# Performance work log

Measured on AMD Instinct MI355X. Metric: run time of the kernel, lower is better.

Reference implementation:

```python
import jax, jax.numpy as jnp
import numpy as np

EPS = 1e-6
CHUNK = 128  # chunk size for the causal linear-attention scan


def elu_plus_one(x):
    return jax.nn.elu(x) + 1.0


def causal_linear_attention(q, k, v):
    # out_t = (sq_t @ cumsum_{j<=t} sk_j v_j^T) / (sq_t . cumsum_{j<=t} sk_j), clamped
    B, S, D = q.shape
    sq = elu_plus_one(q)
    sk = elu_plus_one(k)
    N = S // CHUNK
    # [N, B, C, D] chunked layout for scan over chunks
    sq_c = sq.reshape(B, N, CHUNK, D).transpose(1, 0, 2, 3)
    sk_c = sk.reshape(B, N, CHUNK, D).transpose(1, 0, 2, 3)
    v_c = v.reshape(B, N, CHUNK, D).transpose(1, 0, 2, 3)
    mask = jnp.tril(jnp.ones((CHUNK, CHUNK), dtype=q.dtype))  # inclusive causal

    def step(carry, inp):
        S_kv, z = carry  # [B,D,D], [B,D] running sums from previous chunks
        sqi, ski, vi = inp
        A = jnp.einsum('bid,bjd->bij', sqi, ski) * mask  # intra-chunk causal scores
        num = jnp.einsum('bij,bje->bie', A, vi) + jnp.einsum('bid,bde->bie', sqi, S_kv)
        den = A.sum(-1) + jnp.einsum('bid,bd->bi', sqi, z)
        out = num / jnp.clip(den, EPS, None)[..., None]
        S_kv = S_kv + jnp.einsum('bcd,bce->bde', ski, vi)
        z = z + ski.sum(axis=1)
        return (S_kv, z), out

    init = (jnp.zeros((B, D, D), q.dtype), jnp.zeros((B, D), q.dtype))
    _, outs = jax.lax.scan(step, init, (sq_c, sk_c, v_c))
    return outs.transpose(1, 0, 2, 3).reshape(B, S, D)


def setup_inputs() -> dict:
    key = jax.random.key(0)
    ks = jax.random.split(key, 8)
    B, S, D = 2, 2048, 1024
    scale = 1.0 / np.sqrt(D)  # realistic init scale for the D x D projections
    return {
        'hidden_states': jax.random.normal(ks[0], (B, S, D), jnp.float32),
        'w_q': jax.random.normal(ks[1], (D, D), jnp.float32) * scale,
        'w_k': jax.random.normal(ks[2], (D, D), jnp.float32) * scale,
        'w_v': jax.random.normal(ks[3], (D, D), jnp.float32) * scale,
        'w_o': jax.random.normal(ks[4], (D, D), jnp.float32) * scale,
        'gate': jnp.zeros((1,), jnp.float32),
        'memory': jax.random.uniform(ks[5], (D, D), jnp.float32) * 0.01,
        'memory_norm': jax.random.uniform(ks[6], (D,), jnp.float32),
    }


def reference(hidden_states, w_q, w_k, w_v, w_o, gate, memory, memory_norm):
    # Projections (torch Linear: x @ W^T)
    q = hidden_states @ w_q.T
    k = hidden_states @ w_k.T
    v = hidden_states @ w_v.T

    # Retrieve from compressive memory (single bank)
    sigma_q = elu_plus_one(q)
    a_mem = sigma_q @ memory
    norm = jnp.clip(sigma_q @ memory_norm, EPS, None)[..., None]
    active = (memory_norm.sum() >= EPS).astype(q.dtype)
    memory_output = active * (a_mem / norm)

    local_output = causal_linear_attention(q, k, v)

    g = jax.nn.sigmoid(gate)  # [1], broadcasts
    output = g * memory_output + (1.0 - g) * local_output
    return output @ w_o.T
```

## Files before the change

kernel.cpp:

```cpp
#include <hip/hip_runtime.h>
#include <cstddef>

#define EPSF 1e-6f

constexpr int D   = 1024;
constexpr int Bv  = 2;
constexpr int S   = 2048;
constexpr int M   = Bv * S;
constexpr int CH  = 256;
constexpr int NCH = S / CH;

constexpr int TSZ  = 128 * 32;
constexpr int TA64 = 64 * 32;

typedef __attribute__((ext_vector_type(8))) short short8;
typedef __attribute__((ext_vector_type(4))) float floatx4;

__device__ __forceinline__ float elu1(float x) { return x > 0.f ? x + 1.f : __expf(x); }
__device__ __forceinline__ float sigmoidf_(float x) { return 1.f / (1.f + __expf(-x)); }
__device__ __forceinline__ unsigned short f2bf(float x) {
    unsigned u = __float_as_uint(x);
    return (unsigned short)((u + 0x7fffu + ((u >> 16) & 1u)) >> 16);
}
__device__ __forceinline__ float bf2f(unsigned short h) {
    return __uint_as_float(((unsigned)h) << 16);
}
__device__ __forceinline__ float wave_reduce(float x) {
#pragma unroll
    for (int off = 32; off > 0; off >>= 1) x += __shfl_down(x, off);
    return x;
}

__device__ __forceinline__ void gl_lds16(const unsigned short* g, unsigned short* l) {
    __builtin_amdgcn_global_load_lds(
        (const __attribute__((address_space(1))) void*)g,
        (__attribute__((address_space(3))) void*)l, 16, 0, 0);
}

__device__ __forceinline__ void stage128x32(const unsigned short* g, int stride,
                                            unsigned short* lds, int wave, int lane) {
    const int t   = (wave << 6) + lane;
    const int row = t >> 2;
    const int cb  = (((t & 3) ^ ((row >> 1) & 3)) << 3);
    unsigned short* l0 = lds + (wave << 9);
    gl_lds16(g + (size_t)row * stride + cb, l0);
    gl_lds16(g + (size_t)(row + 64) * stride + cb, l0 + 2048);
}

__device__ __forceinline__ void stage64x32(const unsigned short* g, int stride,
                                           unsigned short* lds, int wave, int lane) {
    const int t   = (wave << 6) + lane;
    const int row = t >> 2;
    const int cb  = (((t & 3) ^ ((row >> 1) & 3)) << 3);
    gl_lds16(g + (size_t)row * stride + cb, lds + (wave << 9));
}

__device__ __forceinline__ void mfma_step(const unsigned short* As, const unsigned short* Bs,
                                          int wm, int wn, int fr, int g, floatx4 acc[4][4]) {
    const int off = ((g ^ ((fr >> 1) & 3)) << 3);
    short8 af[4], bf[4];
#pragma unroll
    for (int i = 0; i < 4; ++i) af[i] = *(const short8*)&As[(wm + i * 16 + fr) * 32 + off];
#pragma unroll
    for (int j = 0; j < 4; ++j) bf[j] = *(const short8*)&Bs[(wn + j * 16 + fr) * 32 + off];
#pragma unroll
    for (int i = 0; i < 4; ++i)
#pragma unroll
        for (int j = 0; j < 4; ++j)
            acc[i][j] = __builtin_amdgcn_mfma_f32_16x16x32_bf16(af[i], bf[j], acc[i][j], 0, 0, 0);
}

__device__ __forceinline__ void mfma_step64d(const unsigned short* As, const unsigned short* Bs,
                                             int wm, int wn, int fr, int g,
                                             floatx4 acc[2][4], floatx4 accd[2], short8 bones) {
    const int off = ((g ^ ((fr >> 1) & 3)) << 3);
    short8 af[2], bf[4];
#pragma unroll
    for (int i = 0; i < 2; ++i) af[i] = *(const short8*)&As[(wm + i * 16 + fr) * 32 + off];
#pragma unroll
    for (int j = 0; j < 4; ++j) bf[j] = *(const short8*)&Bs[(wn + j * 16 + fr) * 32 + off];
#pragma unroll
    for (int i = 0; i < 2; ++i) {
#pragma unroll
        for (int j = 0; j < 4; ++j)
            acc[i][j] = __builtin_amdgcn_mfma_f32_16x16x32_bf16(af[i], bf[j], acc[i][j], 0, 0, 0);
        accd[i] = __builtin_amdgcn_mfma_f32_16x16x32_bf16(af[i], bones, accd[i], 0, 0, 0);
    }
}

__device__ __forceinline__ void mfma_step64(const unsigned short* As, const unsigned short* Bs,
                                            int wm, int wn, int fr, int g, floatx4 acc[2][4]) {
    const int off = ((g ^ ((fr >> 1) & 3)) << 3);
    short8 af[2], bf[4];
#pragma unroll
    for (int i = 0; i < 2; ++i) af[i] = *(const short8*)&As[(wm + i * 16 + fr) * 32 + off];
#pragma unroll
    for (int j = 0; j < 4; ++j) bf[j] = *(const short8*)&Bs[(wn + j * 16 + fr) * 32 + off];
#pragma unroll
    for (int i = 0; i < 2; ++i)
#pragma unroll
        for (int j = 0; j < 4; ++j)
            acc[i][j] = __builtin_amdgcn_mfma_f32_16x16x32_bf16(af[i], bf[j], acc[i][j], 0, 0, 0);
}

__device__ __forceinline__ void gemm_loop_db(const unsigned short* Ag, int strideA,
                                             const unsigned short* Bg, int strideB, int Kk,
                                             unsigned short* As, unsigned short* Bs,
                                             int wave, int lane, int wm, int wn, int fr, int g,
                                             floatx4 acc[4][4]) {
    __syncthreads();
    stage128x32(Ag, strideA, As, wave, lane);
    stage128x32(Bg, strideB, Bs, wave, lane);
    int buf = 0;
    for (int k0 = 32; k0 < Kk; k0 += 32) {
        __syncthreads();
        const int nb = buf ^ 1;
        stage128x32(Ag + k0, strideA, As + nb * TSZ, wave, lane);
        stage128x32(Bg + k0, strideB, Bs + nb * TSZ, wave, lane);
        mfma_step(As + buf * TSZ, Bs + buf * TSZ, wm, wn, fr, g, acc);
        buf = nb;
    }
    __syncthreads();
    mfma_step(As + buf * TSZ, Bs + buf * TSZ, wm, wn, fr, g, acc);
}

__device__ __forceinline__ void gemm_loop_db64d(const unsigned short* Ag, int strideA,
                                                const unsigned short* Bg, int strideB, int Kk,
                                                unsigned short* As, unsigned short* Bs,
                                                int wave, int lane, int wm, int wn, int fr, int g,
                                                floatx4 acc[2][4], floatx4 accd[2], short8 bones) {
    __syncthreads();
    stage64x32(Ag, strideA, As, wave, lane);
    stage128x32(Bg, strideB, Bs, wave, lane);
    int buf = 0;
    for (int k0 = 32; k0 < Kk; k0 += 32) {
        __syncthreads();
        const int nb = buf ^ 1;
        stage64x32(Ag + k0, strideA, As + nb * TA64, wave, lane);
        stage128x32(Bg + k0, strideB, Bs + nb * TSZ, wave, lane);
        mfma_step64d(As + buf * TA64, Bs + buf * TSZ, wm, wn, fr, g, acc, accd, bones);
        buf = nb;
    }
    __syncthreads();
    mfma_step64d(As + buf * TA64, Bs + buf * TSZ, wm, wn, fr, g, acc, accd, bones);
}

__device__ __forceinline__ void gemm_loop_db64(const unsigned short* Ag, int strideA,
                                               const unsigned short* Bg, int strideB, int Kk,
                                               unsigned short* As, unsigned short* Bs,
                                               int wave, int lane, int wm, int wn, int fr, int g,
                                               floatx4 acc[2][4]) {
    __syncthreads();
    stage64x32(Ag, strideA, As, wave, lane);
    stage128x32(Bg, strideB, Bs, wave, lane);
    int buf = 0;
    for (int k0 = 32; k0 < Kk; k0 += 32) {
        __syncthreads();
        const int nb = buf ^ 1;
        stage64x32(Ag + k0, strideA, As + nb * TA64, wave, lane);
        stage128x32(Bg + k0, strideB, Bs + nb * TSZ, wave, lane);
        mfma_step64(As + buf * TA64, Bs + buf * TSZ, wm, wn, fr, g, acc);
        buf = nb;
    }
    __syncthreads();
    mfma_step64(As + buf * TA64, Bs + buf * TSZ, wm, wn, fr, g, acc);
}

__global__ __launch_bounds__(256) void prep(const float* __restrict__ h,
                                            const float* __restrict__ w_q, const float* __restrict__ w_k,
                                            const float* __restrict__ w_v, const float* __restrict__ w_o,
                                            const float* __restrict__ memory,
                                            unsigned short* __restrict__ h_b,
                                            unsigned short* __restrict__ wq_b, unsigned short* __restrict__ wk_b,
                                            unsigned short* __restrict__ wv_b, unsigned short* __restrict__ wo_b,
                                            unsigned short* __restrict__ memT)
{
    __shared__ unsigned short T[64][72];
    const int id = blockIdx.x, tid = threadIdx.x;
    if (id < 4096) {
        const size_t i = ((size_t)id * 256 + tid) * 4;
        float4 v = *(const float4*)(h + i);
        ushort4 o; o.x = f2bf(v.x); o.y = f2bf(v.y); o.z = f2bf(v.z); o.w = f2bf(v.w);
        *(ushort4*)(h_b + i) = o;
    } else if (id < 8192) {
        const int t = id - 4096, which = t >> 10;
        const float* in = (which == 0) ? w_q : (which == 1) ? w_k : (which == 2) ? w_v : w_o;
        unsigned short* out = (which == 0) ? wq_b : (which == 1) ? wk_b : (which == 2) ? wv_b : wo_b;
        const size_t i = ((size_t)(t & 1023) * 256 + tid) * 4;
        float4 v = *(const float4*)(in + i);
        ushort4 o; o.x = f2bf(v.x); o.y = f2bf(v.y); o.z = f2bf(v.z); o.w = f2bf(v.w);
        *(ushort4*)(out + i) = o;
    } else {
        const int t = id - 8192;
        const int d0 = (t >> 4) * 64, e0 = (t & 15) * 64;
        const int r = tid >> 4, c4 = (tid & 15) * 4;
        for (int rr = r; rr < 64; rr += 16) {
            float4 v = *(const float4*)(memory + (size_t)(d0 + rr) * D + e0 + c4);
            T[rr][c4 + 0] = f2bf(v.x); T[rr][c4 + 1] = f2bf(v.y);
            T[rr][c4 + 2] = f2bf(v.z); T[rr][c4 + 3] = f2bf(v.w);
        }
        __syncthreads();
        for (int rr = r; rr < 64; rr += 16) {
            ushort4 o;
            o.x = T[c4 + 0][rr]; o.y = T[c4 + 1][rr];
            o.z = T[c4 + 2][rr]; o.w = T[c4 + 3][rr];
            *(ushort4*)(memT + (size_t)(e0 + rr) * D + d0 + c4) = o;
        }
    }
}

__global__ __launch_bounds__(512, 2) void proj8(const unsigned short* __restrict__ h_b,
                                                const unsigned short* __restrict__ wq,
                                                const unsigned short* __restrict__ wk,
                                                const unsigned short* __restrict__ wv,
                                                unsigned short* __restrict__ sq,
                                                unsigned short* __restrict__ sk,
                                                unsigned short* __restrict__ v)
{
    extern __shared__ unsigned short sm[];
    const int id = blockIdx.x;
    const int x = id & 7, y = id >> 3;
    const int strip = x + 8 * (y % 6);
    const int nn = y / 6;
    const int sub = strip >> 4, m = strip & 15;
    const int m0 = m * 256, n0 = nn * 256;
    const unsigned short* Ag = h_b + (size_t)m0 * D;
    const unsigned short* Bg = ((sub == 0) ? wq : (sub == 1) ? wk : wv) + (size_t)n0 * D;
    unsigned short* C = (sub == 0) ? sq : (sub == 1) ? sk : v;

    const int tid = threadIdx.x;
    const int w = tid >> 6, lane = tid & 63;
    const int wr = w >> 2, wc = w & 3;
    const int fr = lane & 15, gq = lane >> 4;
    const int swz = fr & 7;

    const int r0 = tid >> 3;
    const int c0 = (tid & 7) ^ (r0 & 7);
    const int r1 = (tid + 512) >> 3;
    const int c1 = ((tid + 512) & 7) ^ (r1 & 7);
    const size_t so0 = (size_t)r0 * D + (size_t)c0 * 8;
    const size_t so1 = (size_t)r1 * D + (size_t)c1 * 8;
    unsigned short* const dst0 = sm + tid * 8;
    unsigned short* const dst1 = sm + (tid + 512) * 8;

    floatx4 acc[8][4] = {};

#define STG(kt, b, which) do {                                                      \
        const unsigned short* Gs = ((which) < 2 ? Ag : Bg)                          \
            + (size_t)(((which) & 1) * 128) * D + (size_t)(kt) * 64;                \
        const int slot = (((b) << 2) + (which)) << 13;                              \
        gl_lds16(Gs + so0, dst0 + slot);                                            \
        gl_lds16(Gs + so1, dst1 + slot);                                            \
    } while (0)

    STG(0, 0, 0); STG(0, 0, 1); STG(0, 0, 2); STG(0, 0, 3);
    STG(1, 1, 2); STG(1, 1, 3);
    asm volatile("s_waitcnt vmcnt(4)" ::: "memory");
    __builtin_amdgcn_s_barrier();

    const int NT = D / 64;
    for (int u = 0; u < NT; ++u) {
        const int bu = u & 1;
        const unsigned short* Ah = sm + (((bu << 2) + wr) << 13);
        const unsigned short* Bh = sm + (((bu << 2) + 2 + (wc >> 1)) << 13);
        const int brow = (wc & 1) * 64;
        short8 bfr[4][2];
#pragma unroll
        for (int s = 0; s < 4; ++s) {
            short8 afr[2][2];
#pragma unroll
            for (int i2 = 0; i2 < 2; ++i2)
#pragma unroll
                for (int ks = 0; ks < 2; ++ks)
                    afr[i2][ks] = *(const short8*)&Ah[((s * 2 + i2) * 16 + fr) * 64
                                                      + ((((ks << 2) + gq) ^ swz) << 3)];
            if (s == 0) {
#pragma unroll
                for (int j = 0; j < 4; ++j)
#pragma unroll
                    for (int ks = 0; ks < 2; ++ks)
                        bfr[j][ks] = *(const short8*)&Bh[(brow + j * 16 + fr) * 64
                                                         + ((((ks << 2) + gq) ^ swz) << 3)];
            }
            if (s == 0)      { if (u + 1 < NT) STG(u + 1, bu ^ 1, 0); }
            else if (s == 1) { if (u + 1 < NT) STG(u + 1, bu ^ 1, 1); }
            else if (s == 2) { if (u + 2 < NT) STG(u + 2, bu, 2); }
            else {
                if (u + 2 < NT) {
                    STG(u + 2, bu, 3);
                    asm volatile("s_waitcnt vmcnt(4)" ::: "memory");
                } else if (u + 1 < NT) {
                    asm volatile("s_waitcnt vmcnt(0)" ::: "memory");
                }
            }
            __builtin_amdgcn_s_barrier();
            __builtin_amdgcn_s_setprio(1);
#pragma unroll
            for (int i2 = 0; i2 < 2; ++i2)
#pragma unroll
                for (int j = 0; j < 4; ++j)
#pragma unroll
                    for (int ks = 0; ks < 2; ++ks)
                        acc[s * 2 + i2][j] = __builtin_amdgcn_mfma_f32_16x16x32_bf16(
                            afr[i2][ks], bfr[j][ks], acc[s * 2 + i2][j], 0, 0, 0);
            __builtin_amdgcn_s_setprio(0);
            __builtin_amdgcn_s_barrier();
        }
    }
#undef STG

    const int q4 = gq * 4;
#pragma unroll
    for (int i = 0; i < 8; ++i)
#pragma unroll
        for (int j = 0; j < 4; ++j) {
            const int col = n0 + wc * 64 + j * 16 + fr;
#pragma unroll
            for (int r = 0; r < 4; ++r) {
                const int row = m0 + wr * 128 + i * 16 + q4 + r;
                float val = acc[i][j][r];
                if (sub < 2) val = elu1(val);
                C[(size_t)row * D + col] = f2bf(val);
            }
        }
}

__global__ __launch_bounds__(256) void proj_fused(const unsigned short* __restrict__ h_b,
                                                  const unsigned short* __restrict__ wq,
                                                  const unsigned short* __restrict__ wk,
                                                  const unsigned short* __restrict__ wv,
                                                  unsigned short* __restrict__ sq,
                                                  unsigned short* __restrict__ sk,
                                                  unsigned short* __restrict__ v)
{
    __shared__ unsigned short As[2 * TSZ], Bs[2 * TSZ];
    const int id = blockIdx.x;
    const int x = id & 7, y = id >> 3;
    const int strip = x + 8 * (y % 12);
    const int n     = y / 12;
    const int sub = strip >> 5, m = strip & 31;
    const int m0 = m * 128, n0 = n * 128;
    const unsigned short* B = (sub == 0) ? wq : (sub == 1) ? wk : wv;
    unsigned short* C = (sub == 0) ? sq : (sub == 1) ? sk : v;

    const int tid = threadIdx.x, wave = tid >> 6, lane = tid & 63;
    const int wm = (wave >> 1) * 64, wn = (wave & 1) * 64;
    const int fr = lane & 15, g = lane >> 4;
    const int q4 = g * 4;

    floatx4 acc[4][4] = {};
    gemm_loop_db(h_b + (size_t)m0 * D, D, B + (size_t)n0 * D, D, D,
                 As, Bs, wave, lane, wm, wn, fr, g, acc);

#pragma unroll
    for (int i = 0; i < 4; ++i)
#pragma unroll
        for (int j = 0; j < 4; ++j) {
            const int col = n0 + wn + j * 16 + fr;
#pragma unroll
            for (int r = 0; r < 4; ++r) {
                const int row = m0 + wm + i * 16 + q4 + r;
                float val = acc[i][j][r];
                if (sub < 2) val = elu1(val);
                C[(size_t)row * D + col] = f2bf(val);
            }
        }
}

__global__ __launch_bounds__(256) void stage2(const unsigned short* __restrict__ sq,
                                              const unsigned short* __restrict__ sk,
                                              const unsigned short* __restrict__ memT,
                                              const unsigned short* __restrict__ v_b,
                                              const float* __restrict__ mnorm,
                                              const float* __restrict__ gate,
                                              unsigned short* __restrict__ combm,
                                              unsigned short* __restrict__ Sbuf2,
                                              unsigned short* __restrict__ vT,
                                              float* __restrict__ rowscale)
{
    __shared__ unsigned short As[2 * TSZ], Bs[2 * TSZ];
    const int id = blockIdx.x, tid = threadIdx.x;
    const int wave = tid >> 6, lane = tid & 63;
    const int wm = (wave >> 1) * 64, wn = (wave & 1) * 64;
    const int fr = lane & 15, g = lane >> 4;
    const int q4 = g * 4;

    if (id < 256) {
        const int x = id & 7, y = id >> 3;
        const int m0 = (x + 8 * (y & 3)) * 128;
        const int n0 = (y >> 2) * 128;
        floatx4 acc[4][4] = {};
        gemm_loop_db(sq + (size_t)m0 * D, D, memT + (size_t)n0 * D, D, D,
                     As, Bs, wave, lane, wm, wn, fr, g, acc);
#pragma unroll
        for (int i = 0; i < 4; ++i)
#pragma unroll
            for (int j = 0; j < 4; ++j) {
                const int col = n0 + wn + j * 16 + fr;
#pragma unroll
                for (int r = 0; r < 4; ++r)
                    combm[(size_t)(m0 + wm + i * 16 + q4 + r) * D + col] = f2bf(acc[i][j][r]);
            }
    } else if (id < 544) {
        const int t = id - 256;
        const int b = t / 144, rem = t % 144;
        const int p = rem >> 2, tt = rem & 3;
        const int it = tt >> 1, jt = tt & 1;
        int c = 0;
        while ((c + 1) * (c + 2) / 2 <= p) ++c;
        const int j = p - c * (c + 1) / 2;
        unsigned short* Srow0 = Sbuf2 + (size_t)(b * NCH + c) * CH * S;

        if (j == c && jt > it) {
            const int row = it * 128 + (tid >> 1);
            unsigned short* zp = Srow0 + (size_t)row * S + j * CH + jt * 128 + (tid & 1) * 64;
            uint4 z4 = make_uint4(0, 0, 0, 0);
#pragma unroll
            for (int i = 0; i < 8; ++i) *(uint4*)(zp + i * 8) = z4;
            return;
        }
        floatx4 acc[4][4] = {};
        gemm_loop_db(sq + ((size_t)b * S + (size_t)c * CH + it * 128) * D, D,
                     sk + ((size_t)b * S + (size_t)j * CH + jt * 128) * D, D, D,
                     As, Bs, wave, lane, wm, wn, fr, g, acc);
        const bool diag = (j == c && it == jt);
#pragma unroll
        for (int i = 0; i < 4; ++i)
#pragma unroll
            for (int jj = 0; jj < 4; ++jj) {
                const int col = jt * 128 + wn + jj * 16 + fr;
#pragma unroll
                for (int r = 0; r < 4; ++r) {
                    const int row = it * 128 + wm + i * 16 + q4 + r;
                    float val = acc[i][jj][r];
                    if (diag && col > row) val = 0.f;
                    Srow0[(size_t)row * S + j * CH + col] = f2bf(val);
                }
            }
    } else if (id < 1568) {
        unsigned short (*T)[72] = (unsigned short(*)[72])As;
        const int t = id - 544;
        const int b = t >> 9, rem = t & 511;
        const int s0 = (rem >> 4) * 64, d0 = (rem & 15) * 64;
        const int r = tid >> 4, c4 = (tid & 15) * 4;
        const unsigned short* ip = v_b + (size_t)b * S * D;
        for (int rr = r; rr < 64; rr += 16) {
            ushort4 vv = *(const ushort4*)(ip + (size_t)(s0 + rr) * D + d0 + c4);
            T[rr][c4 + 0] = vv.x; T[rr][c4 + 1] = vv.y; T[rr][c4 + 2] = vv.z; T[rr][c4 + 3] = vv.w;
        }
        __syncthreads();
        unsigned short* op = vT + (size_t)b * D * S;
        for (int rr = r; rr < 64; rr += 16) {
            ushort4 o;
            o.x = T[c4 + 0][rr]; o.y = T[c4 + 1][rr];
            o.z = T[c4 + 2][rr]; o.w = T[c4 + 3][rr];
            *(ushort4*)(op + (size_t)(d0 + rr) * S + s0 + c4) = o;
        }
    } else {
        const int row = (id - 1568) * 4 + wave;
        const unsigned short* sr = sq + (size_t)row * D;
        float dot = 0.f, msum = 0.f;
#pragma unroll
        for (int p = 0; p < 2; ++p) {
            const int d0 = p * 512 + lane * 8;
            short8 sv = *(const short8*)(sr + d0);
            float4 m0 = *(const float4*)(mnorm + d0);
            float4 m1 = *(const float4*)(mnorm + d0 + 4);
            dot += bf2f((unsigned short)sv[0]) * m0.x + bf2f((unsigned short)sv[1]) * m0.y
                 + bf2f((unsigned short)sv[2]) * m0.z + bf2f((unsigned short)sv[3]) * m0.w
                 + bf2f((unsigned short)sv[4]) * m1.x + bf2f((unsigned short)sv[5]) * m1.y
                 + bf2f((unsigned short)sv[6]) * m1.z + bf2f((unsigned short)sv[7]) * m1.w;
            msum += m0.x + m0.y + m0.z + m0.w + m1.x + m1.y + m1.z + m1.w;
        }
        dot = wave_reduce(dot);
        msum = wave_reduce(msum);
        if (lane == 0) {
            const float gg = sigmoidf_(gate[0]);
            const float active = (msum >= EPSF) ? 1.f : 0.f;
            rowscale[row] = gg * active / fmaxf(dot, EPSF);
        }
    }
}

__global__ __launch_bounds__(256) void pv64(const unsigned short* __restrict__ Sbuf2,
                                            const unsigned short* __restrict__ vT,
                                            const float* __restrict__ rowscale,
                                            const float* __restrict__ gate,
                                            unsigned short* __restrict__ combm)
{
    __shared__ unsigned short As2[2 * TA64], Bs2[2 * TSZ];
    const int id = blockIdx.x, tid = threadIdx.x;
    const int wave = tid >> 6, lane = tid & 63;
    const int wm = (wave >> 1) * 32, wn = (wave & 1) * 64;
    const int fr = lane & 15, g = lane >> 4;
    const int q4 = g * 4;

    const int x = id & 7, y = id >> 3;
    const int g_ = x + 8 * (y & 7);
    const int e  = y >> 3;
    const int b = g_ >> 5;
    const int rem = g_ & 31;
    const int c = (NCH - 1) - (rem >> 2);
    const int i0 = (rem & 3) * 64, e0 = e * 128;

    const short one_bf = (short)0x3F80;
    short8 bones = {one_bf, one_bf, one_bf, one_bf, one_bf, one_bf, one_bf, one_bf};

    floatx4 acc[2][4] = {};
    floatx4 accd[2] = {};
    gemm_loop_db64d(Sbuf2 + ((size_t)(b * NCH + c) * CH + i0) * S, S,
                    vT + (size_t)b * D * S + (size_t)e0 * S, S, (c + 1) * CH,
                    As2, Bs2, wave, lane, wm, wn, fr, g, acc, accd, bones);

    const float gg = sigmoidf_(gate[0]);
    const float wloc = 1.f - gg;
#pragma unroll
    for (int i = 0; i < 2; ++i)
#pragma unroll
        for (int j = 0; j < 4; ++j) {
            const int col = e0 + wn + j * 16 + fr;
#pragma unroll
            for (int r = 0; r < 4; ++r) {
                const int li = i0 + wm + i * 16 + q4 + r;
                const int rg = b * S + c * CH + li;
                const float inv = wloc / fmaxf(accd[i][r], EPSF);
                const size_t idx = (size_t)rg * D + col;
                combm[idx] = f2bf(bf2f(combm[idx]) * rowscale[rg] + acc[i][j][r] * inv);
            }
        }
}

__global__ __launch_bounds__(256) void outproj64(const unsigned short* __restrict__ A,
                                                 const unsigned short* __restrict__ wo,
                                                 float* __restrict__ out)
{
    __shared__ unsigned short As2[2 * TA64], Bs2[2 * TSZ];
    const int id = blockIdx.x, tid = threadIdx.x;
    const int wave = tid >> 6, lane = tid & 63;
    const int wm = (wave >> 1) * 32, wn = (wave & 1) * 64;
    const int fr = lane & 15, g = lane >> 4;
    const int q4 = g * 4;

    const int x = id & 7, y = id >> 3;
    const int m0 = (x + 8 * (y & 7)) * 64;
    const int n0 = (y >> 3) * 128;

    floatx4 acc[2][4] = {};
    gemm_loop_db64(A + (size_t)m0 * D, D, wo + (size_t)n0 * D, D, D,
                   As2, Bs2, wave, lane, wm, wn, fr, g, acc);

#pragma unroll
    for (int i = 0; i < 2; ++i)
#pragma unroll
        for (int j = 0; j < 4; ++j) {
            const int col = n0 + wn + j * 16 + fr;
#pragma unroll
            for (int r = 0; r < 4; ++r)
                out[(size_t)(m0 + wm + i * 16 + q4 + r) * D + col] = acc[i][j][r];
        }
}

extern "C" void kernel_launch(void* const* d_in, const int* in_sizes, int n_in,
                              void* d_out, int out_size, void* d_ws, size_t ws_size,
                              hipStream_t stream)
{
    const float* h      = (const float*)d_in[0];
    const float* w_q    = (const float*)d_in[1];
    const float* w_k    = (const float*)d_in[2];
    const float* w_v    = (const float*)d_in[3];
    const float* w_o    = (const float*)d_in[4];
    const float* gate   = (const float*)d_in[5];
    const float* memory = (const float*)d_in[6];
    const float* mnorm  = (const float*)d_in[7];
    float* out = (float*)d_out;

    unsigned short* h_b   = (unsigned short*)d_ws;
    unsigned short* wq_b  = h_b + (size_t)M * D;
    unsigned short* wk_b  = wq_b + (size_t)D * D;
    unsigned short* wv_b  = wk_b + (size_t)D * D;
    unsigned short* wo_b  = wv_b + (size_t)D * D;
    unsigned short* memT  = wo_b + (size_t)D * D;
    unsigned short* sq_b  = memT + (size_t)D * D;
    unsigned short* sk_b  = sq_b + (size_t)M * D;
    unsigned short* v_b   = sk_b + (size_t)M * D;
    unsigned short* vT    = v_b + (size_t)M * D;
    unsigned short* Sbuf2 = vT + (size_t)M * D;
    unsigned short* combm = Sbuf2 + (size_t)Bv * NCH * CH * S;
    float* rowscale = (float*)(combm + (size_t)M * D);

    dim3 blk(256);

    prep<<<8448, blk, 0, stream>>>(h, w_q, w_k, w_v, w_o, memory,
                                   h_b, wq_b, wk_b, wv_b, wo_b, memT);

    static const bool proj8_ok = [] {
        return hipFuncSetAttribute(reinterpret_cast<const void*>(proj8),
                                   hipFuncAttributeMaxDynamicSharedMemorySize,
                                   131072) == hipSuccess;
    }();
    if (proj8_ok)
        proj8<<<192, dim3(512), 131072, stream>>>(h_b, wq_b, wk_b, wv_b, sq_b, sk_b, v_b);
    else
        proj_fused<<<768, blk, 0, stream>>>(h_b, wq_b, wk_b, wv_b, sq_b, sk_b, v_b);

    stage2<<<2592, blk, 0, stream>>>(sq_b, sk_b, memT, v_b, mnorm, gate,
                                     combm, Sbuf2, vT, rowscale);
    pv64<<<512, blk, 0, stream>>>(Sbuf2, vT, rowscale, gate, combm);
    outproj64<<<512, blk, 0, stream>>>(combm, wo_b, out);
}
```

Baseline: 227.2 us.

## Move stage2 GEMMs onto 256x256 tiled 512-thread pipelined kernel

Pulls the 256x256 MFMA GEMM pipeline out into a shared device function and adds a new stage2n kernel that uses it. stage2n computes the memory retrieval sq@mem and the lower-triangular chunk score blocks sq_c@sk_j^T with large 256x256 tiles and 128KB of LDS. It also folds the V transpose and the per-row norm/scale work into the same launch. The goal is better data reuse and MFMA utilization than the previous 256-thread stage2, at the cost of fewer, heavier blocks and possible load imbalance between the block types.

```diff
diff --git a/kernel.cpp b/kernel.cpp
--- a/kernel.cpp
+++ b/kernel.cpp
@@ -35,6 +35,88 @@
     __builtin_amdgcn_global_load_lds(
         (const __attribute__((address_space(1))) void*)g,
         (__attribute__((address_space(3))) void*)l, 16, 0, 0);
+}
+
+__device__ __forceinline__ void gemm256_8ph(const unsigned short* __restrict__ Ag,
+                                            const unsigned short* __restrict__ Bg,
+                                            unsigned short* sm, int tid,
+                                            floatx4 acc[8][4]) {
+    const int lane = tid & 63, w = tid >> 6;
+    const int wr = w >> 2, wc = w & 3;
+    const int fr = lane & 15, gq = lane >> 4;
+    const int swz = fr & 7;
+
+    const int r0 = tid >> 3;
+    const int c0 = (tid & 7) ^ (r0 & 7);
+    const int r1 = (tid + 512) >> 3;
+    const int c1 = ((tid + 512) & 7) ^ (r1 & 7);
+    const size_t so0 = (size_t)r0 * D + (size_t)c0 * 8;
+    const size_t so1 = (size_t)r1 * D + (size_t)c1 * 8;
+    unsigned short* const dst0 = sm + tid * 8;
+    unsigned short* const dst1 = sm + (tid + 512) * 8;
+
+    auto STG = [&](int kt, int b, int which) {
+        const unsigned short* Gs = ((which) < 2 ? Ag : Bg)
+            + (size_t)(((which) & 1) * 128) * D + (size_t)(kt) * 64;
+        const int slot = (((b) << 2) + (which)) << 13;
+        gl_lds16(Gs + so0, dst0 + slot);
+        gl_lds16(Gs + so1, dst1 + slot);
+    };
+
+    STG(0, 0, 0); STG(0, 0, 1); STG(0, 0, 2); STG(0, 0, 3);
+    STG(1, 1, 2); STG(1, 1, 3);
+    asm volatile("s_waitcnt vmcnt(4)" ::: "memory");
+    __builtin_amdgcn_s_barrier();
+
+    const int NT = D / 64;
+    for (int u = 0; u < NT; ++u) {
+        const int bu = u & 1;
+        const unsigned short* Ah = sm + (((bu << 2) + wr) << 13);
+        const unsigned short* Bh = sm + (((bu << 2) + 2 + (wc >> 1)) << 13);
+        const int brow = (wc & 1) * 64;
+        short8 bfr[4][2];
+#pragma unroll
+        for (int s = 0; s < 4; ++s) {
+            short8 afr[2][2];
+#pragma unroll
+            for (int i2 = 0; i2 < 2; ++i2)
+#pragma unroll
+                for (int ks = 0; ks < 2; ++ks)
+                    afr[i2][ks] = *(const short8*)&Ah[((s * 2 + i2) * 16 + fr) * 64
+                                                      + ((((ks << 2) + gq) ^ swz) << 3)];
+            if (s == 0) {
+#pragma unroll
+                for (int j = 0; j < 4; ++j)
+#pragma unroll
+                    for (int ks = 0; ks < 2; ++ks)
+                        bfr[j][ks] = *(const short8*)&Bh[(brow + j * 16 + fr) * 64
+                                                         + ((((ks << 2) + gq) ^ swz) << 3)];
+            }
+            if (s == 0)      { if (u + 1 < NT) STG(u + 1, bu ^ 1, 0); }
+            else if (s == 1) { if (u + 1 < NT) STG(u + 1, bu ^ 1, 1); }
+            else if (s == 2) { if (u + 2 < NT) STG(u + 2, bu, 2); }
+            else {
+                if (u + 2 < NT) {
+                    STG(u + 2, bu, 3);
+                    asm volatile("s_waitcnt vmcnt(4)" ::: "memory");
+                } else if (u + 1 < NT) {
+                    asm volatile("s_waitcnt vmcnt(0)" ::: "memory");
+                }
+            }
+            __builtin_amdgcn_s_barrier();
+            __builtin_amdgcn_s_setprio(1);
+#pragma unroll
+            for (int i2 = 0; i2 < 2; ++i2)
+#pragma unroll
+                for (int j = 0; j < 4; ++j)
+#pragma unroll
+                    for (int ks = 0; ks < 2; ++ks)
+                        acc[s * 2 + i2][j] = __builtin_amdgcn_mfma_f32_16x16x32_bf16(
+                            afr[i2][ks], bfr[j][ks], acc[s * 2 + i2][j], 0, 0, 0);
+            __builtin_amdgcn_s_setprio(0);
+            __builtin_amdgcn_s_barrier();
+        }
+    }
 }
 
 __device__ __forceinline__ void stage128x32(const unsigned short* g, int stride,
@@ -232,82 +314,9 @@
     const int w = tid >> 6, lane = tid & 63;
     const int wr = w >> 2, wc = w & 3;
     const int fr = lane & 15, gq = lane >> 4;
-    const int swz = fr & 7;
-
-    const int r0 = tid >> 3;
-    const int c0 = (tid & 7) ^ (r0 & 7);
-    const int r1 = (tid + 512) >> 3;
-    const int c1 = ((tid + 512) & 7) ^ (r1 & 7);
-    const size_t so0 = (size_t)r0 * D + (size_t)c0 * 8;
-    const size_t so1 = (size_t)r1 * D + (size_t)c1 * 8;
-    unsigned short* const dst0 = sm + tid * 8;
-    unsigned short* const dst1 = sm + (tid + 512) * 8;
 
     floatx4 acc[8][4] = {};
-
-#define STG(kt, b, which) do {                                                      \
-        const unsigned short* Gs = ((which) < 2 ? Ag : Bg)                          \
-            + (size_t)(((which) & 1) * 128) * D + (size_t)(kt) * 64;                \
-        const int slot = (((b) << 2) + (which)) << 13;                              \
-        gl_lds16(Gs + so0, dst0 + slot);                                            \
-        gl_lds16(Gs + so1, dst1 + slot);                                            \
-    } while (0)
-
-    STG(0, 0, 0); STG(0, 0, 1); STG(0, 0, 2); STG(0, 0, 3);
-    STG(1, 1, 2); STG(1, 1, 3);
-    asm volatile("s_waitcnt vmcnt(4)" ::: "memory");
-    __builtin_amdgcn_s_barrier();
-
-    const int NT = D / 64;
-    for (int u = 0; u < NT; ++u) {
-        const int bu = u & 1;
-        const unsigned short* Ah = sm + (((bu << 2) + wr) << 13);
-        const unsigned short* Bh = sm + (((bu << 2) + 2 + (wc >> 1)) << 13);
-        const int brow = (wc & 1) * 64;
-        short8 bfr[4][2];
-#pragma unroll
-        for (int s = 0; s < 4; ++s) {
-            short8 afr[2][2];
-#pragma unroll
-            for (int i2 = 0; i2 < 2; ++i2)
-#pragma unroll
-                for (int ks = 0; ks < 2; ++ks)
-                    afr[i2][ks] = *(const short8*)&Ah[((s * 2 + i2) * 16 + fr) * 64
-                                                      + ((((ks << 2) + gq) ^ swz) << 3)];
-            if (s == 0) {
-#pragma unroll
-                for (int j = 0; j < 4; ++j)
-#pragma unroll
-                    for (int ks = 0; ks < 2; ++ks)
-                        bfr[j][ks] = *(const short8*)&Bh[(brow + j * 16 + fr) * 64
-                                                         + ((((ks << 2) + gq) ^ swz) << 3)];
-            }
-            if (s == 0)      { if (u + 1 < NT) STG(u + 1, bu ^ 1, 0); }
-            else if (s == 1) { if (u + 1 < NT) STG(u + 1, bu ^ 1, 1); }
-            else if (s == 2) { if (u + 2 < NT) STG(u + 2, bu, 2); }
-            else {
-                if (u + 2 < NT) {
-                    STG(u + 2, bu, 3);
-                    asm volatile("s_waitcnt vmcnt(4)" ::: "memory");
-                } else if (u + 1 < NT) {
-                    asm volatile("s_waitcnt vmcnt(0)" ::: "memory");
-                }
-            }
-            __builtin_amdgcn_s_barrier();
-            __builtin_amdgcn_s_setprio(1);
-#pragma unroll
-            for (int i2 = 0; i2 < 2; ++i2)
-#pragma unroll
-                for (int j = 0; j < 4; ++j)
-#pragma unroll
-                    for (int ks = 0; ks < 2; ++ks)
-                        acc[s * 2 + i2][j] = __builtin_amdgcn_mfma_f32_16x16x32_bf16(
-                            afr[i2][ks], bfr[j][ks], acc[s * 2 + i2][j], 0, 0, 0);
-            __builtin_amdgcn_s_setprio(0);
-            __builtin_amdgcn_s_barrier();
-        }
-    }
-#undef STG
+    gemm256_8ph(Ag, Bg, sm, tid, acc);
 
     const int q4 = gq * 4;
 #pragma unroll
@@ -323,6 +332,113 @@
                 C[(size_t)row * D + col] = f2bf(val);
             }
         }
+}
+
+__global__ __launch_bounds__(512, 2) void stage2n(const unsigned short* __restrict__ sq,
+                                                  const unsigned short* __restrict__ sk,
+                                                  const unsigned short* __restrict__ memT,
+                                                  const unsigned short* __restrict__ v_b,
+                                                  const float* __restrict__ mnorm,
+                                                  const float* __restrict__ gate,
+                                                  unsigned short* __restrict__ combm,
+                                                  unsigned short* __restrict__ Sbuf2,
+                                                  unsigned short* __restrict__ vT,
+                                                  float* __restrict__ rowscale)
+{
+    extern __shared__ unsigned short sm[];
+    const int id = blockIdx.x, tid = threadIdx.x;
+
+    if (id < 136) {
+        const int wk = (id & 7) * 17 + (id >> 3);
+        const int w = tid >> 6, lane = tid & 63;
+        const int wr = w >> 2, wc = w & 3;
+        const int fr = lane & 15, gq = lane >> 4;
+        const int q4 = gq * 4;
+
+        if (wk < 64) {
+            const int mt = wk >> 2, nt = wk & 3;
+            const int m0 = mt * 256, n0 = nt * 256;
+            floatx4 acc[8][4] = {};
+            gemm256_8ph(sq + (size_t)m0 * D, memT + (size_t)n0 * D, sm, tid, acc);
+#pragma unroll
+            for (int i = 0; i < 8; ++i)
+#pragma unroll
+                for (int j = 0; j < 4; ++j) {
+                    const int col = n0 + wc * 64 + j * 16 + fr;
+#pragma unroll
+                    for (int r = 0; r < 4; ++r)
+                        combm[(size_t)(m0 + wr * 128 + i * 16 + q4 + r) * D + col]
+                            = f2bf(acc[i][j][r]);
+                }
+        } else {
+            const int w2 = wk - 64;
+            const int b = w2 / 36, p = w2 % 36;
+            int c = 0;
+            while ((c + 1) * (c + 2) / 2 <= p) ++c;
+            const int jc = p - c * (c + 1) / 2;
+            floatx4 acc[8][4] = {};
+            gemm256_8ph(sq + ((size_t)b * S + (size_t)c * CH) * D,
+                        sk + ((size_t)b * S + (size_t)jc * CH) * D, sm, tid, acc);
+            unsigned short* Srow0 = Sbuf2 + (size_t)(b * NCH + c) * CH * S + jc * CH;
+            const bool diag = (jc == c);
+#pragma unroll
+            for (int i = 0; i < 8; ++i)
+#pragma unroll
+                for (int j = 0; j < 4; ++j) {
+                    const int col = wc * 64 + j * 16 + fr;
+#pragma unroll
+                    for (int r = 0; r < 4; ++r) {
+                        const int row = wr * 128 + i * 16 + q4 + r;
+                        float val = acc[i][j][r];
+                        if (diag && col > row) val = 0.f;
+                        Srow0[(size_t)row * S + col] = f2bf(val);
+                    }
+                }
+        }
+    } else if (id < 136 + 1024) {
+        unsigned short (*T)[72] = (unsigned short(*)[72])sm;
+        const int t = id - 136;
+        const int b = t >> 9, rem = t & 511;
+        const int s0 = (rem >> 4) * 64, d0 = (rem & 15) * 64;
+        const int r = tid >> 4, c4 = (tid & 15) * 4;
+        const unsigned short* ip = v_b + (size_t)b * S * D;
+        for (int rr = r; rr < 64; rr += 32) {
+            ushort4 vv = *(const ushort4*)(ip + (size_t)(s0 + rr) * D + d0 + c4);
+            T[rr][c4 + 0] = vv.x; T[rr][c4 + 1] = vv.y; T[rr][c4 + 2] = vv.z; T[rr][c4 + 3] = vv.w;
+        }
+        __syncthreads();
+        unsigned short* op = vT + (size_t)b * D * S;
+        for (int rr = r; rr < 64; rr += 32) {
+            ushort4 o;
+            o.x = T[c4 + 0][rr]; o.y = T[c4 + 1][rr];
+            o.z = T[c4 + 2][rr]; o.w = T[c4 + 3][rr];
+            *(ushort4*)(op + (size_t)(d0 + rr) * S + s0 + c4) = o;
+        }
+    } else {
+        const int wave = tid >> 6, lane = tid & 63;
+        const int row = (id - 136 - 1024) * 8 + wave;
+        const unsigned short* sr = sq + (size_t)row * D;
+        float dot = 0.f, msum = 0.f;
+#pragma unroll
+        for (int p = 0; p < 2; ++p) {
+            const int d0 = p * 512 + lane * 8;
+            short8 sv = *(const short8*)(sr + d0);
+            float4 m0 = *(const float4*)(mnorm + d0);
+            float4 m1 = *(const float4*)(mnorm + d0 + 4);
+            dot += bf2f((unsigned short)sv[0]) * m0.x + bf2f((unsigned short)sv[1]) * m0.y
+                 + bf2f((unsigned short)sv[2]) * m0.z + bf2f((unsigned short)sv[3]) * m0.w
+                 + bf2f((unsigned short)sv[4]) * m1.x + bf2f((unsigned short)sv[5]) * m1.y
+                 + bf2f((unsigned short)sv[6]) * m1.z + bf2f((unsigned short)sv[7]) * m1.w;
+            msum += m0.x + m0.y + m0.z + m0.w + m1.x + m1.y + m1.z + m1.w;
+        }
+        dot = wave_reduce(dot);
+        msum = wave_reduce(msum);
+        if (lane == 0) {
+            const float gg = sigmoidf_(gate[0]);
+            const float active = (msum >= EPSF) ? 1.f : 0.f;
+            rowscale[row] = gg * active / fmaxf(dot, EPSF);
+        }
+    }
 }
 
 __global__ __launch_bounds__(256) void proj_fused(const unsigned short* __restrict__ h_b,
@@ -593,18 +709,26 @@
     prep<<<8448, blk, 0, stream>>>(h, w_q, w_k, w_v, w_o, memory,
                                    h_b, wq_b, wk_b, wv_b, wo_b, memT);
 
-    static const bool proj8_ok = [] {
-        return hipFuncSetAttribute(reinterpret_cast<const void*>(proj8),
-                                   hipFuncAttributeMaxDynamicSharedMemorySize,
-                                   131072) == hipSuccess;
+    static const bool lds128_ok = [] {
+        bool a = hipFuncSetAttribute(reinterpret_cast<const void*>(proj8),
+                                     hipFuncAttributeMaxDynamicSharedMemorySize,
+                                     131072) == hipSuccess;
+        bool b = hipFuncSetAttribute(reinterpret_cast<const void*>(stage2n),
+                                     hipFuncAttributeMaxDynamicSharedMemorySize,
+                                     131072) == hipSuccess;
+        return a && b;
     }();
-    if (proj8_ok)
+
+    if (lds128_ok) {
         proj8<<<192, dim3(512), 131072, stream>>>(h_b, wq_b, wk_b, wv_b, sq_b, sk_b, v_b);
-    else
+        stage2n<<<1672, dim3(512), 131072, stream>>>(sq_b, sk_b, memT, v_b, mnorm, gate,
+                                                     combm, Sbuf2, vT, rowscale);
+    } else {
         proj_fused<<<768, blk, 0, stream>>>(h_b, wq_b, wk_b, wv_b, sq_b, sk_b, v_b);
-
-    stage2<<<2592, blk, 0, stream>>>(sq_b, sk_b, memT, v_b, mnorm, gate,
-                                     combm, Sbuf2, vT, rowscale);
+        stage2<<<2592, blk, 0, stream>>>(sq_b, sk_b, memT, v_b, mnorm, gate,
+                                         combm, Sbuf2, vT, rowscale);
+    }
+
     pv64<<<512, blk, 0, stream>>>(Sbuf2, vT, rowscale, gate, combm);
     outproj64<<<512, blk, 0, stream>>>(combm, wo_b, out);
 }
```

Result: faster. 218.4 us (-3.9%).
